# Kernel tuning notes

Measured on AMD Instinct MI355X. Metric: run time of the kernel, lower is better.

## Reference

```python
import jax, jax.numpy as jnp
import numpy as np

T = 1.0
N_NEG = 50
NUM_CLASSES = 500  # smoothing denominator K from CrossEntropyLabelSmooth (faithful quirk)
EPS = 0.1

B, C, D = 2048, 65536, 256


def setup_inputs() -> dict:
    key = jax.random.key(0)
    k1, k2, k3 = jax.random.split(key, 3)
    f = jax.random.normal(k1, (B, D), dtype=jnp.float32)
    centers = jax.random.normal(k2, (C, D), dtype=jnp.float32)
    label = jax.random.randint(k3, (B,), 0, C, dtype=jnp.int64)
    return {"f": f, "centers": centers, "label": label}


def reference(f, centers, label):
    b = f.shape[0]
    rows = jnp.arange(b)
    mat = f @ centers.T                              # [B, C] similarity scores
    pos = mat[rows, label][:, None]                  # [B, 1] positive score
    # mask the positive column so top-k picks only negatives
    masked = mat.at[rows, label].set(-jnp.inf)
    neg, _ = jax.lax.top_k(masked, N_NEG)            # [B, N_neg]
    preds = jnp.concatenate([pos, neg], axis=1) / T  # [B, 1 + N_neg]
    log_probs = jax.nn.log_softmax(preds, axis=1)
    # label-smoothed one-hot with target class 0 (the positive)
    onehot = jnp.zeros_like(log_probs).at[:, 0].set(1.0)
    targets = (1.0 - EPS) * onehot + EPS / NUM_CLASSES
    loss = (-targets * log_probs).mean(0).sum()
    return loss
```

## Files before the change

kernel.cpp:

```cpp
#include <hip/hip_runtime.h>
#include <hip/hip_fp16.h>

#define B_ROWS 2048
#define C_COLS 65536
#define D_DIM  256
#define N_NEG  50
#define NTILES (C_COLS / 128)

typedef __attribute__((ext_vector_type(8))) short short8;
typedef __attribute__((ext_vector_type(4))) float floatx4;
typedef __fp16 f16x2 __attribute__((ext_vector_type(2)));

__device__ __forceinline__ ushort f2bf(float f) {
  unsigned u = __float_as_uint(f);
  unsigned r = (u + 0x7FFFu + ((u >> 16) & 1u)) >> 16;
  return (ushort)r;
}

__device__ __forceinline__ uint hmax2(uint a, uint b) {
  union { uint u; f16x2 h; } x, y, r;
  x.u = a; y.u = b;
  r.h = __builtin_elementwise_max(x.h, y.h);
  return r.u;
}

__global__ void cvt_swz(const float* __restrict__ in, ushort* __restrict__ out, int n8) {
  int i = blockIdx.x * blockDim.x + threadIdx.x;
  if (i >= n8) return;
  int row = i >> 5;
  int ka  = i & 31;
  int ktile = ka >> 3, kb = ka & 7;
  const float4* src = (const float4*)(in + (size_t)i * 8);
  float4 a = src[0], b = src[1];
  ushort4 o0, o1;
  o0.x = f2bf(a.x); o0.y = f2bf(a.y); o0.z = f2bf(a.z); o0.w = f2bf(a.w);
  o1.x = f2bf(b.x); o1.y = f2bf(b.y); o1.z = f2bf(b.z); o1.w = f2bf(b.w);
  ushort* dst = out + (size_t)row * D_DIM + ktile * 64 + ((kb ^ (row & 7)) << 3);
  ((ushort4*)dst)[0] = o0;
  ((ushort4*)dst)[1] = o1;
}

__device__ __forceinline__ void async16(const void* g, void* l) {
  __builtin_amdgcn_global_load_lds((const __attribute__((address_space(1))) void*)g,
                                   (__attribute__((address_space(3))) void*)l,
                                   16, 0, 0);
}

template <bool PREB>
__global__ void gemm_reduce(const ushort* __restrict__ fb,
                            const ushort* __restrict__ cb,
                            const float* __restrict__ cen,
                            const int* __restrict__ label,
                            ushort* __restrict__ cand) {
  __shared__ __align__(16) ushort Cs[128 * 64];
  __shared__ __align__(16) ushort Fs[128 * 64];
  __shared__ __align__(16) ushort gm[128][8];
  __shared__ int labLDS[128];

  const int tid = threadIdx.x, wave = tid >> 6, lane = tid & 63;
  const int l = lane & 15, q = lane >> 4;

  const int lin = blockIdx.y * 16 + blockIdx.x;
  const int lg  = (lin & 7) * 1024 + (lin >> 3);
  const int m0 = (lg & 15) << 7;
  const int bxTile = lg >> 4;
  const int n0 = bxTile << 7;
  if (tid < 128) labLDS[tid] = label[m0 + tid];

  floatx4 acc[4][4] = {};
  const int wn = (wave >> 1) * 64, wm = (wave & 1) * 64;

  for (int kt = 0; kt < D_DIM / 64; ++kt) {
#pragma unroll
    for (int r = 0; r < 4; ++r) {
      int idx = r * 2048 + wave * 512 + lane * 8;
      int row = idx >> 6, kk = idx & 63;
      async16(fb + (size_t)(m0 + row) * D_DIM + kt * 64 + kk, Fs + r * 2048 + wave * 512);
      if (PREB)
        async16(cb + (size_t)(n0 + row) * D_DIM + kt * 64 + kk, Cs + r * 2048 + wave * 512);
    }
    if (!PREB) {
      float4 ra[4], rb[4];
#pragma unroll
      for (int g = 0; g < 4; ++g) {
        int e = (tid + g * 256) * 8;
        const float* gp = cen + (size_t)(n0 + (e >> 6)) * D_DIM + kt * 64 + (e & 63);
        ra[g] = *(const float4*)gp;
        rb[g] = *(const float4*)(gp + 4);
      }
#pragma unroll
      for (int g = 0; g < 4; ++g) {
        int e = (tid + g * 256) * 8;
        int row = e >> 6, kblk = (e >> 3) & 7;
        uint4 o;
        o.x = (uint)f2bf(ra[g].x) | ((uint)f2bf(ra[g].y) << 16);
        o.y = (uint)f2bf(ra[g].z) | ((uint)f2bf(ra[g].w) << 16);
        o.z = (uint)f2bf(rb[g].x) | ((uint)f2bf(rb[g].y) << 16);
        o.w = (uint)f2bf(rb[g].z) | ((uint)f2bf(rb[g].w) << 16);
        *(uint4*)(Cs + (row << 6) + ((kblk ^ (row & 7)) << 3)) = o;
      }
    }
    __syncthreads();

#pragma unroll
    for (int ks = 0; ks < 2; ++ks) {
      short8 a[4], b[4];
#pragma unroll
      for (int i = 0; i < 4; ++i) {
        int swz = ((4 * ks + q) ^ (l & 7)) << 3;
        a[i] = *(const short8*)(Cs + ((wn + i * 16 + l) << 6) + swz);
        b[i] = *(const short8*)(Fs + ((wm + i * 16 + l) << 6) + swz);
      }
#pragma unroll
      for (int i = 0; i < 4; ++i)
#pragma unroll
        for (int j = 0; j < 4; ++j)
          acc[i][j] = __builtin_amdgcn_mfma_f32_16x16x32_bf16(a[i], b[j], acc[i][j], 0, 0, 0);
    }
    __syncthreads();
  }

  int lj[4];
#pragma unroll
  for (int j = 0; j < 4; ++j) lj[j] = labLDS[wm + j * 16 + l] - n0 - wn;
  bool hit = false;
#pragma unroll
  for (int j = 0; j < 4; ++j) hit = hit || ((unsigned)lj[j] < 64u);
  if (__any(hit)) {
#pragma unroll
    for (int j = 0; j < 4; ++j) {
      int relq = lj[j] - q * 4;
#pragma unroll
      for (int i = 0; i < 4; ++i) {
        int rel = relq - i * 16;
#pragma unroll
        for (int r = 0; r < 4; ++r)
          if (rel == r) acc[i][j][r] = -INFINITY;
      }
    }
  }
#pragma unroll
  for (int j = 0; j < 4; ++j) {
    float mx[4];
#pragma unroll
    for (int i = 0; i < 4; ++i)
      mx[i] = fmaxf(fmaxf(acc[i][j][0], acc[i][j][1]),
                    fmaxf(acc[i][j][2], acc[i][j][3]));
    union { f16x2 h; uint u; } c0, c1;
    c0.h = __builtin_amdgcn_cvt_pkrtz(mx[0], mx[1]);
    c1.h = __builtin_amdgcn_cvt_pkrtz(mx[2], mx[3]);
    uint u01 = c0.u, u23 = c1.u;
    u01 = hmax2(u01, __shfl_xor(u01, 16));
    u01 = hmax2(u01, __shfl_xor(u01, 32));
    u23 = hmax2(u23, __shfl_xor(u23, 16));
    u23 = hmax2(u23, __shfl_xor(u23, 32));
    if (q == 0) {
      uint2 w; w.x = u01; w.y = u23;
      *(uint2*)&gm[wm + j * 16 + l][wn >> 4] = w;
    }
  }
  __syncthreads();
  if (tid < 128) {
    uint4 w = *(const uint4*)&gm[tid][0];
    *(uint4*)(cand + ((size_t)bxTile * B_ROWS + (m0 + tid)) * 8) = w;
  }
}

__device__ __forceinline__ float dec_key(int k) {
  if (k < 0x0400) return -INFINITY;
  ushort h = (k >= 0x8000) ? (ushort)(k ^ 0x8000) : (ushort)(~k & 0xFFFF);
  __half_raw hr; hr.x = h;
  return __half2float((__half)hr);
}

__global__ void final_select(const ushort* __restrict__ cand, const float* __restrict__ f,
                             const float* __restrict__ cen, const int* __restrict__ label,
                             float* __restrict__ rowloss) {
  __shared__ float sred[8];
  __shared__ int   sint[8];
  const int row = blockIdx.x, tid = threadIdx.x;
  const int lane = tid & 63, wid = tid >> 6;
  const int lab = label[row];

  float v[16];
  const uint4* p = (const uint4*)cand;
#pragma unroll
  for (int g = 0; g < 2; ++g) {
    uint4 u = p[(size_t)(tid + g * 256) * B_ROWS + row];
    union { uint u; f16x2 h; } c;
    c.u = u.x; v[g * 8 + 0] = (float)c.h.x; v[g * 8 + 1] = (float)c.h.y;
    c.u = u.y; v[g * 8 + 2] = (float)c.h.x; v[g * 8 + 3] = (float)c.h.y;
    c.u = u.z; v[g * 8 + 4] = (float)c.h.x; v[g * 8 + 5] = (float)c.h.y;
    c.u = u.w; v[g * 8 + 6] = (float)c.h.x; v[g * 8 + 7] = (float)c.h.y;
  }
  float pv = f[(size_t)row * D_DIM + tid] * cen[(size_t)lab * D_DIM + tid];
  float m = -INFINITY;
#pragma unroll
  for (int k = 0; k < 16; ++k) m = fmaxf(m, v[k]);
#pragma unroll
  for (int o = 32; o > 0; o >>= 1) {
    m = fmaxf(m, __shfl_down(m, o));
    pv += __shfl_down(pv, o);
  }
  if (lane == 0) { sred[wid] = m; sred[4 + wid] = pv; }
  __syncthreads();
  m = fmaxf(fmaxf(sred[0], sred[1]), fmaxf(sred[2], sred[3]));
  const float pos = sred[4] + sred[5] + sred[6] + sred[7];

  __half hm = __float2half(m);
  int hb = (int)(*(ushort*)&hm);
  int km = (m >= 0.f) ? (0x8000 | hb) : (~hb & 0xFFFF);
  int lo = km - 2048, hi = km;
  if (lo < 0x0400) lo = 0x0400;
#pragma unroll
  for (int it = 0; it < 12; ++it) {
    int mid = (lo + hi) >> 1;
    float tau = dec_key(mid);
    int c = 0;
#pragma unroll
    for (int k = 0; k < 16; ++k) c += (v[k] > tau) ? 1 : 0;
#pragma unroll
    for (int o = 32; o > 0; o >>= 1) c += __shfl_down(c, o);
    if (lane == 0) sint[(it & 1) * 4 + wid] = c;
    __syncthreads();
    int base = (it & 1) * 4;
    int tot = sint[base] + sint[base + 1] + sint[base + 2] + sint[base + 3];
    if (tot <= 49) hi = mid; else lo = mid + 1;
  }

  const float tau = dec_key(hi);
  float sum = 0.f, se = 0.f; int c = 0;
#pragma unroll
  for (int k = 0; k < 16; ++k) {
    if (v[k] > tau) { ++c; sum += v[k]; se += expf(v[k] - m); }
  }
#pragma unroll
  for (int o = 32; o > 0; o >>= 1) {
    sum += __shfl_down(sum, o);
    se  += __shfl_down(se, o);
    c   += __shfl_down(c, o);
  }
  if (lane == 0) { sred[wid] = sum; sred[4 + wid] = se; sint[wid] = c; }
  __syncthreads();
  if (tid == 0) {
    float S = sred[0] + sred[1] + sred[2] + sred[3];
    float E = sred[4] + sred[5] + sred[6] + sred[7];
    int   C = sint[0] + sint[1] + sint[2] + sint[3];
    float nfill = (float)(N_NEG - C);
    S += nfill * tau;
    E += nfill * expf(tau - m);
    float M = fmaxf(m, pos);
    float seAll = E * expf(m - M) + expf(pos - M);
    float lse = M + logf(seAll);
    rowloss[row] = 0.9102f * lse - 0.9002f * pos - 2.0e-4f * S;
  }
}

__global__ void sum_loss(const float* __restrict__ rowloss, float* __restrict__ out) {
  __shared__ float red[4];
  const int tid = threadIdx.x;
  float s = 0.f;
  for (int i = tid; i < B_ROWS; i += 256) s += rowloss[i];
#pragma unroll
  for (int o = 32; o > 0; o >>= 1) s += __shfl_down(s, o);
  if ((tid & 63) == 0) red[tid >> 6] = s;
  __syncthreads();
  if (tid == 0) out[0] = (red[0] + red[1] + red[2] + red[3]) * (1.0f / B_ROWS);
}

extern "C" void kernel_launch(void* const* d_in, const int* in_sizes, int n_in,
                              void* d_out, int out_size, void* d_ws, size_t ws_size,
                              hipStream_t stream) {
  const float* f   = (const float*)d_in[0];
  const float* cen = (const float*)d_in[1];
  const int*   label = (const int*)d_in[2];
  float* out = (float*)d_out;

  char* ws = (char*)d_ws;
  ushort* cand    = (ushort*)ws;
  ushort* fb      = (ushort*)(ws + 16777216);
  float*  rowloss = (float*)(ws + 17825792);
  ushort* cb      = (ushort*)(ws + 17833984);
  const bool pre = ws_size >= (17833984ull + 33554432ull);

  cvt_swz<<<256, 256, 0, stream>>>(f, fb, (B_ROWS * D_DIM) / 8);

  dim3 grid(B_ROWS / 128, NTILES);
  if (pre) {
    cvt_swz<<<8192, 256, 0, stream>>>(cen, cb, (C_COLS * D_DIM) / 8);
    gemm_reduce<true><<<grid, 256, 0, stream>>>(fb, cb, nullptr, label, cand);
  } else {
    gemm_reduce<false><<<grid, 256, 0, stream>>>(fb, nullptr, cen, label, cand);
  }

  final_select<<<B_ROWS, 256, 0, stream>>>(cand, f, cen, label, rowloss);
  sum_loss<<<1, 256, 0, stream>>>(rowloss, out);
}
```

Measured before the change: 209.8 us.

## Assign one wavefront per row in final_select with LDS-staged coalesced candidate loads

Restructures final_select so each 512-thread block handles 8 rows, with one wavefront per row. Candidates for the 8 rows are loaded in coalesced 128-byte chunks into a swizzled LDS tile, then each wave reads its row's 64 values per lane. All reductions, including those inside the 12-step threshold binary search, now use wave-level shuffles instead of block-wide __syncthreads. This removes the strided per-row gathers and the block barriers, at the cost of about 64 KB of LDS per block and 64 live float registers per thread.

```diff
diff --git a/kernel.cpp b/kernel.cpp
--- a/kernel.cpp
+++ b/kernel.cpp
@@ -173,82 +173,86 @@
   return __half2float((__half)hr);
 }
 
-__global__ void final_select(const ushort* __restrict__ cand, const float* __restrict__ f,
-                             const float* __restrict__ cen, const int* __restrict__ label,
-                             float* __restrict__ rowloss) {
-  __shared__ float sred[8];
-  __shared__ int   sint[8];
-  const int row = blockIdx.x, tid = threadIdx.x;
-  const int lane = tid & 63, wid = tid >> 6;
+__global__ __launch_bounds__(512) void final_select(const ushort* __restrict__ cand,
+                                                    const float* __restrict__ f,
+                                                    const float* __restrict__ cen,
+                                                    const int* __restrict__ label,
+                                                    float* __restrict__ rowloss) {
+  __shared__ __align__(16) uint4 ST[NTILES][8];
+  const int tid = threadIdx.x;
+  const int lane = tid & 63, w = tid >> 6;
+  const int row0 = blockIdx.x * 8;
+
+  const uint4* p = (const uint4*)cand;
+#pragma unroll
+  for (int k = 0; k < 8; ++k) {
+    int j = k * 512 + tid;
+    int tile = j >> 3, rr = j & 7;
+    ST[tile][rr ^ (tile & 7)] = p[(size_t)tile * B_ROWS + row0 + rr];
+  }
+  __syncthreads();
+
+  const int row = row0 + w;
   const int lab = label[row];
 
-  float v[16];
-  const uint4* p = (const uint4*)cand;
-#pragma unroll
-  for (int g = 0; g < 2; ++g) {
-    uint4 u = p[(size_t)(tid + g * 256) * B_ROWS + row];
-    union { uint u; f16x2 h; } c;
-    c.u = u.x; v[g * 8 + 0] = (float)c.h.x; v[g * 8 + 1] = (float)c.h.y;
-    c.u = u.y; v[g * 8 + 2] = (float)c.h.x; v[g * 8 + 3] = (float)c.h.y;
-    c.u = u.z; v[g * 8 + 4] = (float)c.h.x; v[g * 8 + 5] = (float)c.h.y;
-    c.u = u.w; v[g * 8 + 6] = (float)c.h.x; v[g * 8 + 7] = (float)c.h.y;
-  }
-  float pv = f[(size_t)row * D_DIM + tid] * cen[(size_t)lab * D_DIM + tid];
-  float m = -INFINITY;
-#pragma unroll
-  for (int k = 0; k < 16; ++k) m = fmaxf(m, v[k]);
+  float v[64];
+#pragma unroll
+  for (int c = 0; c < 8; ++c) {
+    int tile = c * 64 + lane;
+    uint4 u = ST[tile][w ^ (tile & 7)];
+    union { uint u; f16x2 h; } cv;
+    cv.u = u.x; v[c * 8 + 0] = (float)cv.h.x; v[c * 8 + 1] = (float)cv.h.y;
+    cv.u = u.y; v[c * 8 + 2] = (float)cv.h.x; v[c * 8 + 3] = (float)cv.h.y;
+    cv.u = u.z; v[c * 8 + 4] = (float)cv.h.x; v[c * 8 + 5] = (float)cv.h.y;
+    cv.u = u.w; v[c * 8 + 6] = (float)cv.h.x; v[c * 8 + 7] = (float)cv.h.y;
+  }
+
+  float4 fv = *(const float4*)(f   + (size_t)row * D_DIM + lane * 4);
+  float4 cv4 = *(const float4*)(cen + (size_t)lab * D_DIM + lane * 4);
+  float pv = fv.x * cv4.x + fv.y * cv4.y + fv.z * cv4.z + fv.w * cv4.w;
+
+  float m = v[0];
+#pragma unroll
+  for (int k = 1; k < 64; ++k) m = fmaxf(m, v[k]);
 #pragma unroll
   for (int o = 32; o > 0; o >>= 1) {
-    m = fmaxf(m, __shfl_down(m, o));
-    pv += __shfl_down(pv, o);
-  }
-  if (lane == 0) { sred[wid] = m; sred[4 + wid] = pv; }
-  __syncthreads();
-  m = fmaxf(fmaxf(sred[0], sred[1]), fmaxf(sred[2], sred[3]));
-  const float pos = sred[4] + sred[5] + sred[6] + sred[7];
+    m = fmaxf(m, __shfl_xor(m, o));
+    pv += __shfl_xor(pv, o);
+  }
+  const float pos = pv;
 
   __half hm = __float2half(m);
   int hb = (int)(*(ushort*)&hm);
   int km = (m >= 0.f) ? (0x8000 | hb) : (~hb & 0xFFFF);
   int lo = km - 2048, hi = km;
   if (lo < 0x0400) lo = 0x0400;
-#pragma unroll
   for (int it = 0; it < 12; ++it) {
     int mid = (lo + hi) >> 1;
     float tau = dec_key(mid);
     int c = 0;
 #pragma unroll
-    for (int k = 0; k < 16; ++k) c += (v[k] > tau) ? 1 : 0;
-#pragma unroll
-    for (int o = 32; o > 0; o >>= 1) c += __shfl_down(c, o);
-    if (lane == 0) sint[(it & 1) * 4 + wid] = c;
-    __syncthreads();
-    int base = (it & 1) * 4;
-    int tot = sint[base] + sint[base + 1] + sint[base + 2] + sint[base + 3];
-    if (tot <= 49) hi = mid; else lo = mid + 1;
+    for (int k = 0; k < 64; ++k) c += (v[k] > tau) ? 1 : 0;
+#pragma unroll
+    for (int o = 32; o > 0; o >>= 1) c += __shfl_xor(c, o);
+    if (c <= 49) hi = mid; else lo = mid + 1;
   }
 
   const float tau = dec_key(hi);
   float sum = 0.f, se = 0.f; int c = 0;
 #pragma unroll
-  for (int k = 0; k < 16; ++k) {
+  for (int k = 0; k < 64; ++k) {
     if (v[k] > tau) { ++c; sum += v[k]; se += expf(v[k] - m); }
   }
 #pragma unroll
   for (int o = 32; o > 0; o >>= 1) {
-    sum += __shfl_down(sum, o);
-    se  += __shfl_down(se, o);
-    c   += __shfl_down(c, o);
-  }
-  if (lane == 0) { sred[wid] = sum; sred[4 + wid] = se; sint[wid] = c; }
-  __syncthreads();
-  if (tid == 0) {
-    float S = sred[0] + sred[1] + sred[2] + sred[3];
-    float E = sred[4] + sred[5] + sred[6] + sred[7];
-    int   C = sint[0] + sint[1] + sint[2] + sint[3];
-    float nfill = (float)(N_NEG - C);
-    S += nfill * tau;
-    E += nfill * expf(tau - m);
+    sum += __shfl_xor(sum, o);
+    se  += __shfl_xor(se, o);
+    c   += __shfl_xor(c, o);
+  }
+  if (lane == 0) {
+    float nfill = (float)(N_NEG - c);
+    float S = sum + nfill * tau;
+    float E = se + nfill * expf(tau - m);
     float M = fmaxf(m, pos);
     float seAll = E * expf(m - M) + expf(pos - M);
     float lse = M + logf(seAll);
@@ -293,6 +297,6 @@
     gemm_reduce<false><<<grid, 256, 0, stream>>>(fb, nullptr, cen, label, cand);
   }
 
-  final_select<<<B_ROWS, 256, 0, stream>>>(cand, f, cen, label, rowloss);
+  final_select<<<B_ROWS / 8, 512, 0, stream>>>(cand, f, cen, label, rowloss);
   sum_loss<<<1, 256, 0, stream>>>(rowloss, out);
 }
```

New measurement: 190.1 us. 1.1x faster.
